# Kernel optimization log

Measured on AMD Instinct MI355X. Metric: run time of the kernel, lower is better.

The kernel has to match this reference:

```python
import jax, jax.numpy as jnp
import numpy as np

N = 100000  # num nodes


def gcn_conv(x, W, b, row, col, dinv):
    # GCNConv (default PyG): h = D^{-1/2}(A+I)D^{-1/2} (x W) + b
    h = x @ W  # [N, out]
    norm = dinv[row] * dinv[col]  # [E] symmetric normalization
    msg = h[row] * norm[:, None]  # gather + scale per edge
    agg = jax.ops.segment_sum(msg, col, num_segments=N)  # scatter-add to targets
    # self-loop contribution: norm_ii = dinv[i]^2
    agg = agg + h * (dinv * dinv)[:, None]
    return agg + b


def setup_inputs() -> dict:
    key = jax.random.key(0)
    ks = jax.random.split(key, 8)
    x = jax.random.normal(ks[0], (N, 1), dtype=jnp.float32)
    edges = jax.random.randint(ks[1], (2, 3200000), 0, N, dtype=jnp.int64)
    # glorot-ish init for weights, zeros for biases (PyG default bias init is zeros)
    W1 = jax.random.normal(ks[2], (1, 128), dtype=jnp.float32) * (1.0 / np.sqrt(1))
    b1 = jnp.zeros((128,), dtype=jnp.float32)
    W2 = jax.random.normal(ks[3], (128, 128), dtype=jnp.float32) * (1.0 / np.sqrt(128))
    b2 = jnp.zeros((128,), dtype=jnp.float32)
    Wl = jax.random.normal(ks[4], (4, 128), dtype=jnp.float32) * (1.0 / np.sqrt(128))
    bl = jnp.zeros((4,), dtype=jnp.float32)
    return {"x": x, "edges": edges, "W1": W1, "b1": b1, "W2": W2, "b2": b2, "Wl": Wl, "bl": bl}


def reference(x, edges, W1, b1, W2, b2, Wl, bl):
    row, col = edges[0], edges[1]  # source -> target
    # degree (with self loops, edge_weight=1) computed on targets
    deg = jax.ops.segment_sum(jnp.ones(row.shape[0], x.dtype), col, num_segments=N) + 1.0
    dinv = deg ** -0.5
    h = gcn_conv(x, W1, b1, row, col, dinv)
    h = jax.nn.relu(h)
    h = gcn_conv(h, W2, b2, row, col, dinv)
    h = jax.nn.relu(h)
    return h @ Wl.T + bl  # [N, 4]
```

## Files before the change

### kernel.cpp

```cpp
#include <hip/hip_runtime.h>
#include <stdint.h>

#define BK    256
#define CAP   10240
#define SLICE 1024
#define NSL   (CAP / SLICE)
#define EPE   32
#define FCH   (EPE * 256)
#define NBMAX 512

__device__ __forceinline__ float bf2f(uint16_t b){
    uint32_t u = ((uint32_t)b) << 16;
    float f; __builtin_memcpy(&f, &u, 4); return f;
}
__device__ __forceinline__ uint16_t f2bf(float f){
    uint32_t u; __builtin_memcpy(&u, &f, 4);
    uint32_t r = u + 0x7FFFu + ((u >> 16) & 1u);
    return (uint16_t)(r >> 16);
}

__global__ void k_setup(const uint32_t* __restrict__ ew, const uint16_t* __restrict__ xw,
                        const void* __restrict__ W1, const void* __restrict__ W2,
                        const void* __restrict__ b2, const void* __restrict__ Wl,
                        const void* __restrict__ bl, int* __restrict__ flg,
                        int* __restrict__ bucket_cur, int nb, float* __restrict__ g){
    int t = threadIdx.x;
    if (blockIdx.x == 0){
        __shared__ uint32_t orv;
        __shared__ int cntv;
        if (t == 0){ orv = 0u; cntv = 0; }
        __syncthreads();
        uint32_t o = 0;
        for (int i = t; i < 2048; i += 256) o |= ew[2*i + 1];
        int c = 0;
        { uint32_t e = (xw[2*t] >> 7) & 0xFFu; if (e >= 118u && e <= 130u) c = 1; }
        atomicOr(&orv, o);
        atomicAdd(&cntv, c);
        __syncthreads();
        if (t == 0){ flg[0] = (orv == 0u) ? 1 : 0; flg[1] = (cntv >= 128) ? 1 : 0; }
        for (int i = t; i < nb; i += 256) bucket_cur[i] = 0;
    } else {
        __shared__ int cntv;
        __shared__ float wp[128], wm[128];
        if (t == 0) cntv = 0;
        __syncthreads();
        int c = 0;
        { uint32_t e = (xw[2*t] >> 7) & 0xFFu; if (e >= 118u && e <= 130u) c = 1; }
        atomicAdd(&cntv, c);
        __syncthreads();
        int bf = (cntv >= 128);
        if (t < 128){
            float w1 = bf ? bf2f(((const uint16_t*)W1)[t]) : ((const float*)W1)[t];
            wp[t] = fmaxf(w1, 0.f);
            wm[t] = fmaxf(-w1, 0.f);
        }
        __syncthreads();
        if (t < 128){
            float g1 = 0.f, g2 = 0.f;
            for (int k = 0; k < 128; ++k){
                float w2 = bf ? bf2f(((const uint16_t*)W2)[k*128 + t]) : ((const float*)W2)[k*128 + t];
                g1 = fmaf(wp[k], w2, g1);
                g2 = fmaf(wm[k], w2, g2);
            }
            g[t]       = g1;
            g[128 + t] = g2;
            g[256 + t] = bf ? bf2f(((const uint16_t*)b2)[t]) : ((const float*)b2)[t];
            #pragma unroll
            for (int m = 0; m < 4; ++m)
                g[384 + m*128 + t] = bf ? bf2f(((const uint16_t*)Wl)[m*128 + t]) : ((const float*)Wl)[m*128 + t];
            if (t < 4)
                g[896 + t] = bf ? bf2f(((const uint16_t*)bl)[t]) : ((const float*)bl)[t];
        }
    }
}

__global__ void __launch_bounds__(256)
k_fill(const int* __restrict__ e32, int E, const int* __restrict__ flg,
       int* __restrict__ bucket_cur, uint32_t* __restrict__ recs, int nb){
    __shared__ int lhist[NBMAX];
    __shared__ int lbase[NBMAX];
    int tid = threadIdx.x;
    int is64 = flg[0];
    int e0 = blockIdx.x * FCH;
    int cnt = min(FCH, E - e0);
    int rr[EPE], cc[EPE];
    #pragma unroll
    for (int k = 0; k < EPE; ++k) cc[k] = -1;
    for (int i = tid; i < nb; i += 256) lhist[i] = 0;
    __syncthreads();

    if (is64 && ((E & 1) == 0) && ((cnt & 1) == 0)){
        #pragma unroll
        for (int k = 0; k < EPE/2; ++k){
            int idx = (k*256 + tid) * 2;
            if (idx < cnt){
                int4 wr = *(const int4*)&e32[2*((long)e0 + idx)];
                int4 wc = *(const int4*)&e32[2*((long)E + e0 + idx)];
                rr[2*k] = wr.x; cc[2*k] = wc.x;
                rr[2*k+1] = wr.z; cc[2*k+1] = wc.z;
            }
        }
    } else if (!is64 && ((E & 3) == 0) && ((cnt & 3) == 0)){
        #pragma unroll
        for (int k = 0; k < EPE/4; ++k){
            int idx = (k*256 + tid) * 4;
            if (idx < cnt){
                int4 wr = *(const int4*)&e32[(long)e0 + idx];
                int4 wc = *(const int4*)&e32[(long)E + e0 + idx];
                rr[4*k]   = wr.x; cc[4*k]   = wc.x;
                rr[4*k+1] = wr.y; cc[4*k+1] = wc.y;
                rr[4*k+2] = wr.z; cc[4*k+2] = wc.z;
                rr[4*k+3] = wr.w; cc[4*k+3] = wc.w;
            }
        }
    } else {
        #pragma unroll
        for (int k = 0; k < EPE; ++k){
            int i = k*256 + tid;
            if (i < cnt){
                long e = (long)e0 + i;
                if (is64){ rr[k] = e32[2*e]; cc[k] = e32[2*((long)E + e)]; }
                else     { rr[k] = e32[e];   cc[k] = e32[(long)E + e];     }
            }
        }
    }
    #pragma unroll
    for (int k = 0; k < EPE; ++k)
        if (cc[k] >= 0) atomicAdd(&lhist[cc[k] >> 8], 1);
    __syncthreads();
    for (int b = tid; b < nb; b += 256){
        int h = lhist[b];
        lbase[b] = h ? atomicAdd(&bucket_cur[b], h) : 0;
    }
    __syncthreads();
    #pragma unroll
    for (int k = 0; k < EPE; ++k){
        int c = cc[k];
        if (c >= 0){
            int b = c >> 8;
            int slot = atomicAdd(&lbase[b], 1);
            if (slot < CAP)
                recs[(long)b*CAP + slot] = (uint32_t)rr[k] | ((uint32_t)(c & 255) << 20);
        }
    }
}

__global__ void __launch_bounds__(256)
k_deg(const uint32_t* __restrict__ recs, const int* __restrict__ bucket_cur,
      int* __restrict__ degp){
    __shared__ int hist[BK];
    int bs = blockIdx.x, b = bs / NSL, s = bs - b*NSL, tid = threadIdx.x;
    hist[tid] = 0;
    __syncthreads();
    int m = min(bucket_cur[b], CAP);
    int lo = s * SLICE, hi = min(lo + SLICE, m);
    if (lo < hi){
        const uint32_t* rb = recs + (long)b*CAP;
        int i = lo + tid*4;
        uint4 w = *(const uint4*)&rb[i];
        if (i   < hi) atomicAdd(&hist[w.x >> 20], 1);
        if (i+1 < hi) atomicAdd(&hist[w.y >> 20], 1);
        if (i+2 < hi) atomicAdd(&hist[w.z >> 20], 1);
        if (i+3 < hi) atomicAdd(&hist[w.w >> 20], 1);
    }
    __syncthreads();
    degp[(long)bs*BK + tid] = hist[tid];
}

__global__ void k_node1(const int* __restrict__ degp, const void* __restrict__ x,
                        const int* __restrict__ flg, float* __restrict__ darr,
                        float* __restrict__ xdarr, int N){
    int i = blockIdx.x * blockDim.x + threadIdx.x;
    if (i >= N) return;
    int b = i >> 8, lane = i & 255;
    int cnt = 0;
    #pragma unroll
    for (int s = 0; s < NSL; ++s) cnt += degp[((long)b*NSL + s)*BK + lane];
    float d = rsqrtf((float)cnt + 1.0f);
    float xv = flg[1] ? bf2f(((const uint16_t*)x)[i]) : ((const float*)x)[i];
    darr[i]  = d;
    xdarr[i] = xv * d;
}

__global__ void __launch_bounds__(256)
k_sagg(const uint32_t* __restrict__ recs, const int* __restrict__ bucket_cur,
       const float* __restrict__ xdarr, float* __restrict__ saggp){
    __shared__ float acc[BK];
    int bs = blockIdx.x, b = bs / NSL, s = bs - b*NSL, tid = threadIdx.x;
    acc[tid] = 0.f;
    __syncthreads();
    int m = min(bucket_cur[b], CAP);
    int lo = s * SLICE, hi = min(lo + SLICE, m);
    if (lo < hi){
        const uint32_t* rb = recs + (long)b*CAP;
        int i = lo + tid*4;
        uint4 w = *(const uint4*)&rb[i];
        float v0 = xdarr[w.x & 0xFFFFFu];
        float v1 = xdarr[w.y & 0xFFFFFu];
        float v2 = xdarr[w.z & 0xFFFFFu];
        float v3 = xdarr[w.w & 0xFFFFFu];
        if (i   < hi) atomicAdd(&acc[w.x >> 20], v0);
        if (i+1 < hi) atomicAdd(&acc[w.y >> 20], v1);
        if (i+2 < hi) atomicAdd(&acc[w.z >> 20], v2);
        if (i+3 < hi) atomicAdd(&acc[w.w >> 20], v3);
    }
    __syncthreads();
    saggp[(long)bs*BK + tid] = acc[tid];
}

__global__ void k_node2(const float* __restrict__ saggp, const float* __restrict__ darr,
                        const float* __restrict__ xdarr, float2* __restrict__ pqd, int N){
    int i = blockIdx.x * blockDim.x + threadIdx.x;
    if (i >= N) return;
    int b = i >> 8, lane = i & 255;
    float sum = 0.f;
    #pragma unroll
    for (int s = 0; s < NSL; ++s) sum += saggp[((long)b*NSL + s)*BK + lane];
    float d = darr[i];
    float sv = d * (sum + xdarr[i]);
    pqd[i] = make_float2(fmaxf(sv, 0.f) * d, fmaxf(-sv, 0.f) * d);
}

__global__ void __launch_bounds__(256)
k_pq(const uint32_t* __restrict__ recs, const int* __restrict__ bucket_cur,
     const float2* __restrict__ pqd, float2* __restrict__ pqp){
    __shared__ float P[BK], Q[BK];
    int bs = blockIdx.x, b = bs / NSL, s = bs - b*NSL, tid = threadIdx.x;
    P[tid] = 0.f; Q[tid] = 0.f;
    __syncthreads();
    int m = min(bucket_cur[b], CAP);
    int lo = s * SLICE, hi = min(lo + SLICE, m);
    if (lo < hi){
        const uint32_t* rb = recs + (long)b*CAP;
        int i = lo + tid*4;
        uint4 w = *(const uint4*)&rb[i];
        float2 v0 = pqd[w.x & 0xFFFFFu];
        float2 v1 = pqd[w.y & 0xFFFFFu];
        float2 v2 = pqd[w.z & 0xFFFFFu];
        float2 v3 = pqd[w.w & 0xFFFFFu];
        if (i   < hi){ atomicAdd(&P[w.x >> 20], v0.x); atomicAdd(&Q[w.x >> 20], v0.y); }
        if (i+1 < hi){ atomicAdd(&P[w.y >> 20], v1.x); atomicAdd(&Q[w.y >> 20], v1.y); }
        if (i+2 < hi){ atomicAdd(&P[w.z >> 20], v2.x); atomicAdd(&Q[w.z >> 20], v2.y); }
        if (i+3 < hi){ atomicAdd(&P[w.w >> 20], v3.x); atomicAdd(&Q[w.w >> 20], v3.y); }
    }
    __syncthreads();
    pqp[(long)bs*BK + tid] = make_float2(P[tid], Q[tid]);
}

__global__ void __launch_bounds__(256)
k_final(const float2* __restrict__ pqp, const float* __restrict__ darr,
        const float2* __restrict__ pqd, const float* __restrict__ g,
        const int* __restrict__ flg, void* __restrict__ out, int N){
    __shared__ float G[900];
    for (int i = threadIdx.x; i < 900; i += 256) G[i] = g[i];
    __syncthreads();
    int i = blockIdx.x * blockDim.x + threadIdx.x;
    if (i >= N) return;
    int b = i >> 8, lane = i & 255;
    float P = 0.f, Q = 0.f;
    #pragma unroll
    for (int s = 0; s < NSL; ++s){
        float2 v = pqp[((long)b*NSL + s)*BK + lane];
        P += v.x; Q += v.y;
    }
    float d = darr[i];
    float2 self = pqd[i];
    float U = d * (P + self.x);
    float V = d * (Q + self.y);
    float o0 = G[896], o1 = G[897], o2 = G[898], o3 = G[899];
    #pragma unroll 4
    for (int j = 0; j < 128; ++j){
        float h = fmaxf(fmaf(U, G[j], fmaf(V, G[128 + j], G[256 + j])), 0.f);
        o0 = fmaf(h, G[384 + j], o0);
        o1 = fmaf(h, G[512 + j], o1);
        o2 = fmaf(h, G[640 + j], o2);
        o3 = fmaf(h, G[768 + j], o3);
    }
    if (flg[1]){
        uint32_t lo = (uint32_t)f2bf(o0) | ((uint32_t)f2bf(o1) << 16);
        uint32_t hi = (uint32_t)f2bf(o2) | ((uint32_t)f2bf(o3) << 16);
        ((uint2*)out)[i] = make_uint2(lo, hi);
    } else {
        ((float4*)out)[i] = make_float4(o0, o1, o2, o3);
    }
}

extern "C" void kernel_launch(void* const* d_in, const int* in_sizes, int n_in,
                              void* d_out, int out_size, void* d_ws, size_t ws_size,
                              hipStream_t stream){
    const int N = in_sizes[0];
    const int E = in_sizes[1] / 2;
    const void* x  = d_in[0];
    const int* e32 = (const int*)d_in[1];
    const void* W1 = d_in[2];
    const void* W2 = d_in[4];
    const void* b2 = d_in[5];
    const void* Wl = d_in[6];
    const void* bl = d_in[7];

    const int NB  = (N + BK - 1) / BK;
    const int nbF = (E + FCH - 1) / FCH;
    const int nb  = (N + 255) / 256;

    char* base = (char*)d_ws;
    size_t off = 0;
    auto alloc = [&](size_t bytes) -> void* {
        void* p = base + off;
        off = (off + bytes + 255) & ~(size_t)255;
        return p;
    };
    int*      flg        = (int*)     alloc(256);
    float*    g          = (float*)   alloc(1024 * 4);
    int*      bucket_cur = (int*)     alloc((size_t)NB * 4);
    float*    darr       = (float*)   alloc((size_t)N * 4);
    float*    xdarr      = (float*)   alloc((size_t)N * 4);
    float2*   pqd        = (float2*)  alloc((size_t)N * 8);
    uint32_t* recs       = (uint32_t*)alloc((size_t)NB * CAP * 4);
    int*      degp       = (int*)     alloc((size_t)NB * NSL * BK * 4);
    float*    saggp      = (float*)   alloc((size_t)NB * NSL * BK * 4);
    float2*   pqp        = (float2*)  alloc((size_t)NB * NSL * BK * 8);
    (void)ws_size; (void)n_in; (void)out_size;

    k_setup <<<2,        256, 0, stream>>>((const uint32_t*)d_in[1], (const uint16_t*)x,
                                           W1, W2, b2, Wl, bl, flg, bucket_cur, NB, g);
    k_fill  <<<nbF,      256, 0, stream>>>(e32, E, flg, bucket_cur, recs, NB);
    k_deg   <<<NB * NSL, 256, 0, stream>>>(recs, bucket_cur, degp);
    k_node1 <<<nb,       256, 0, stream>>>(degp, x, flg, darr, xdarr, N);
    k_sagg  <<<NB * NSL, 256, 0, stream>>>(recs, bucket_cur, xdarr, saggp);
    k_node2 <<<nb,       256, 0, stream>>>(saggp, darr, xdarr, pqd, N);
    k_pq    <<<NB * NSL, 256, 0, stream>>>(recs, bucket_cur, pqd, pqp);
    k_final <<<nb,       256, 0, stream>>>(pqp, darr, pqd, g, flg, d_out, N);
}
```

Measured before the change: 209.3 us.

## Regroup bucket records by source chunk and stage gathers through LDS

Adds a regroup pass that sorts each target bucket's edge records by source-node chunk of 2048 and fuses the degree histogram and dinv computation into it. The aggregation kernels then loop over source chunks, load each chunk of xdarr/pqd into shared memory and gather from LDS instead of doing random global loads. They also fold the per-slice partial sums and node epilogues into the same kernel. This drops several kernels and partial-sum buffers, but adds a full extra read/write of the records. It also serializes the work: each block handles two buckets and iterates over all 49 chunks, so parallelism drops to about 196 blocks, which may underfill the GPU.

```diff
diff --git a/kernel.cpp b/kernel.cpp
--- a/kernel.cpp
+++ b/kernel.cpp
@@ -3,11 +3,11 @@
 
 #define BK    256
 #define CAP   10240
-#define SLICE 1024
-#define NSL   (CAP / SLICE)
 #define EPE   32
 #define FCH   (EPE * 256)
 #define NBMAX 512
+#define CH    2048
+#define NQMAX 64
 
 __device__ __forceinline__ float bf2f(uint16_t b){
     uint32_t u = ((uint32_t)b) << 16;
@@ -146,142 +146,150 @@
 }
 
 __global__ void __launch_bounds__(256)
-k_deg(const uint32_t* __restrict__ recs, const int* __restrict__ bucket_cur,
-      int* __restrict__ degp){
-    __shared__ int hist[BK];
-    int bs = blockIdx.x, b = bs / NSL, s = bs - b*NSL, tid = threadIdx.x;
-    hist[tid] = 0;
+k_regroup(const uint32_t* __restrict__ recs, const int* __restrict__ bucket_cur,
+          const void* __restrict__ x, const int* __restrict__ flg,
+          uint32_t* __restrict__ recs2, int* __restrict__ binoff,
+          float* __restrict__ darr, float* __restrict__ xdarr, int N, int nq){
+    __shared__ int hist[NQMAX];
+    __shared__ int base[NQMAX + 1];
+    __shared__ int dhist[BK];
+    int b = blockIdx.x, tid = threadIdx.x;
+    if (tid < nq) hist[tid] = 0;
+    dhist[tid] = 0;
     __syncthreads();
     int m = min(bucket_cur[b], CAP);
-    int lo = s * SLICE, hi = min(lo + SLICE, m);
-    if (lo < hi){
-        const uint32_t* rb = recs + (long)b*CAP;
-        int i = lo + tid*4;
-        uint4 w = *(const uint4*)&rb[i];
-        if (i   < hi) atomicAdd(&hist[w.x >> 20], 1);
-        if (i+1 < hi) atomicAdd(&hist[w.y >> 20], 1);
-        if (i+2 < hi) atomicAdd(&hist[w.z >> 20], 1);
-        if (i+3 < hi) atomicAdd(&hist[w.w >> 20], 1);
-    }
-    __syncthreads();
-    degp[(long)bs*BK + tid] = hist[tid];
-}
-
-__global__ void k_node1(const int* __restrict__ degp, const void* __restrict__ x,
-                        const int* __restrict__ flg, float* __restrict__ darr,
-                        float* __restrict__ xdarr, int N){
-    int i = blockIdx.x * blockDim.x + threadIdx.x;
-    if (i >= N) return;
-    int b = i >> 8, lane = i & 255;
-    int cnt = 0;
-    #pragma unroll
-    for (int s = 0; s < NSL; ++s) cnt += degp[((long)b*NSL + s)*BK + lane];
-    float d = rsqrtf((float)cnt + 1.0f);
-    float xv = flg[1] ? bf2f(((const uint16_t*)x)[i]) : ((const float*)x)[i];
-    darr[i]  = d;
-    xdarr[i] = xv * d;
+    const uint32_t* rb = recs + (long)b*CAP;
+    for (int i = tid; i < m; i += 256){
+        uint32_t rec = rb[i];
+        atomicAdd(&hist[(rec & 0xFFFFFu) >> 11], 1);
+        atomicAdd(&dhist[rec >> 20], 1);
+    }
+    __syncthreads();
+    if (tid == 0){
+        int s = 0;
+        for (int q = 0; q < nq; ++q){ base[q] = s; s += hist[q]; }
+        base[nq] = s;
+    }
+    __syncthreads();
+    if (tid <= nq) binoff[b*(nq+1) + tid] = base[tid];
+    if (tid < nq)  hist[tid] = base[tid];
+    __syncthreads();
+    for (int i = tid; i < m; i += 256){
+        uint32_t rec = rb[i];
+        int slot = atomicAdd(&hist[(rec & 0xFFFFFu) >> 11], 1);
+        recs2[(long)b*CAP + slot] = rec;
+    }
+    int node = b*BK + tid;
+    if (node < N){
+        float d = rsqrtf((float)dhist[tid] + 1.0f);
+        float xv = flg[1] ? bf2f(((const uint16_t*)x)[node]) : ((const float*)x)[node];
+        darr[node]  = d;
+        xdarr[node] = xv * d;
+    }
 }
 
 __global__ void __launch_bounds__(256)
-k_sagg(const uint32_t* __restrict__ recs, const int* __restrict__ bucket_cur,
-       const float* __restrict__ xdarr, float* __restrict__ saggp){
-    __shared__ float acc[BK];
-    int bs = blockIdx.x, b = bs / NSL, s = bs - b*NSL, tid = threadIdx.x;
-    acc[tid] = 0.f;
-    __syncthreads();
-    int m = min(bucket_cur[b], CAP);
-    int lo = s * SLICE, hi = min(lo + SLICE, m);
-    if (lo < hi){
-        const uint32_t* rb = recs + (long)b*CAP;
-        int i = lo + tid*4;
-        uint4 w = *(const uint4*)&rb[i];
-        float v0 = xdarr[w.x & 0xFFFFFu];
-        float v1 = xdarr[w.y & 0xFFFFFu];
-        float v2 = xdarr[w.z & 0xFFFFFu];
-        float v3 = xdarr[w.w & 0xFFFFFu];
-        if (i   < hi) atomicAdd(&acc[w.x >> 20], v0);
-        if (i+1 < hi) atomicAdd(&acc[w.y >> 20], v1);
-        if (i+2 < hi) atomicAdd(&acc[w.z >> 20], v2);
-        if (i+3 < hi) atomicAdd(&acc[w.w >> 20], v3);
-    }
-    __syncthreads();
-    saggp[(long)bs*BK + tid] = acc[tid];
-}
-
-__global__ void k_node2(const float* __restrict__ saggp, const float* __restrict__ darr,
-                        const float* __restrict__ xdarr, float2* __restrict__ pqd, int N){
-    int i = blockIdx.x * blockDim.x + threadIdx.x;
-    if (i >= N) return;
-    int b = i >> 8, lane = i & 255;
-    float sum = 0.f;
-    #pragma unroll
-    for (int s = 0; s < NSL; ++s) sum += saggp[((long)b*NSL + s)*BK + lane];
-    float d = darr[i];
-    float sv = d * (sum + xdarr[i]);
-    pqd[i] = make_float2(fmaxf(sv, 0.f) * d, fmaxf(-sv, 0.f) * d);
+k_sagg(const uint32_t* __restrict__ recs2, const int* __restrict__ binoff,
+       const float* __restrict__ darr, const float* __restrict__ xdarr,
+       float2* __restrict__ pqd, int N, int nq, int nb){
+    __shared__ float slice[CH];
+    __shared__ float acc[2*BK];
+    int tid = threadIdx.x;
+    int b0 = blockIdx.x * 2;
+    acc[tid] = 0.f; acc[BK + tid] = 0.f;
+    for (int q = 0; q < nq; ++q){
+        __syncthreads();
+        #pragma unroll
+        for (int j = tid; j < CH; j += 256){
+            int gidx = q*CH + j;
+            slice[j] = (gidx < N) ? xdarr[gidx] : 0.f;
+        }
+        __syncthreads();
+        #pragma unroll
+        for (int bb = 0; bb < 2; ++bb){
+            int b = b0 + bb;
+            if (b >= nb) break;
+            int s0 = binoff[b*(nq+1) + q], s1 = binoff[b*(nq+1) + q + 1];
+            const uint32_t* rbase = recs2 + (long)b*CAP;
+            for (int i = s0 + tid; i < s1; i += 256){
+                uint32_t rec = rbase[i];
+                atomicAdd(&acc[bb*BK + (rec >> 20)], slice[rec & (CH-1)]);
+            }
+        }
+    }
+    __syncthreads();
+    #pragma unroll
+    for (int bb = 0; bb < 2; ++bb){
+        int node = (b0 + bb)*BK + tid;
+        if (node < N){
+            float d = darr[node];
+            float sv = d * (acc[bb*BK + tid] + xdarr[node]);
+            pqd[node] = make_float2(fmaxf(sv, 0.f) * d, fmaxf(-sv, 0.f) * d);
+        }
+    }
 }
 
 __global__ void __launch_bounds__(256)
-k_pq(const uint32_t* __restrict__ recs, const int* __restrict__ bucket_cur,
-     const float2* __restrict__ pqd, float2* __restrict__ pqp){
-    __shared__ float P[BK], Q[BK];
-    int bs = blockIdx.x, b = bs / NSL, s = bs - b*NSL, tid = threadIdx.x;
-    P[tid] = 0.f; Q[tid] = 0.f;
-    __syncthreads();
-    int m = min(bucket_cur[b], CAP);
-    int lo = s * SLICE, hi = min(lo + SLICE, m);
-    if (lo < hi){
-        const uint32_t* rb = recs + (long)b*CAP;
-        int i = lo + tid*4;
-        uint4 w = *(const uint4*)&rb[i];
-        float2 v0 = pqd[w.x & 0xFFFFFu];
-        float2 v1 = pqd[w.y & 0xFFFFFu];
-        float2 v2 = pqd[w.z & 0xFFFFFu];
-        float2 v3 = pqd[w.w & 0xFFFFFu];
-        if (i   < hi){ atomicAdd(&P[w.x >> 20], v0.x); atomicAdd(&Q[w.x >> 20], v0.y); }
-        if (i+1 < hi){ atomicAdd(&P[w.y >> 20], v1.x); atomicAdd(&Q[w.y >> 20], v1.y); }
-        if (i+2 < hi){ atomicAdd(&P[w.z >> 20], v2.x); atomicAdd(&Q[w.z >> 20], v2.y); }
-        if (i+3 < hi){ atomicAdd(&P[w.w >> 20], v3.x); atomicAdd(&Q[w.w >> 20], v3.y); }
-    }
-    __syncthreads();
-    pqp[(long)bs*BK + tid] = make_float2(P[tid], Q[tid]);
-}
-
-__global__ void __launch_bounds__(256)
-k_final(const float2* __restrict__ pqp, const float* __restrict__ darr,
-        const float2* __restrict__ pqd, const float* __restrict__ g,
-        const int* __restrict__ flg, void* __restrict__ out, int N){
+k_pqfin(const uint32_t* __restrict__ recs2, const int* __restrict__ binoff,
+        const float* __restrict__ darr, const float2* __restrict__ pqd,
+        const float* __restrict__ g, const int* __restrict__ flg,
+        void* __restrict__ out, int N, int nq, int nb){
+    __shared__ float2 slice[CH];
+    __shared__ float P[2*BK], Q[2*BK];
     __shared__ float G[900];
-    for (int i = threadIdx.x; i < 900; i += 256) G[i] = g[i];
-    __syncthreads();
-    int i = blockIdx.x * blockDim.x + threadIdx.x;
-    if (i >= N) return;
-    int b = i >> 8, lane = i & 255;
-    float P = 0.f, Q = 0.f;
-    #pragma unroll
-    for (int s = 0; s < NSL; ++s){
-        float2 v = pqp[((long)b*NSL + s)*BK + lane];
-        P += v.x; Q += v.y;
-    }
-    float d = darr[i];
-    float2 self = pqd[i];
-    float U = d * (P + self.x);
-    float V = d * (Q + self.y);
-    float o0 = G[896], o1 = G[897], o2 = G[898], o3 = G[899];
-    #pragma unroll 4
-    for (int j = 0; j < 128; ++j){
-        float h = fmaxf(fmaf(U, G[j], fmaf(V, G[128 + j], G[256 + j])), 0.f);
-        o0 = fmaf(h, G[384 + j], o0);
-        o1 = fmaf(h, G[512 + j], o1);
-        o2 = fmaf(h, G[640 + j], o2);
-        o3 = fmaf(h, G[768 + j], o3);
-    }
-    if (flg[1]){
-        uint32_t lo = (uint32_t)f2bf(o0) | ((uint32_t)f2bf(o1) << 16);
-        uint32_t hi = (uint32_t)f2bf(o2) | ((uint32_t)f2bf(o3) << 16);
-        ((uint2*)out)[i] = make_uint2(lo, hi);
-    } else {
-        ((float4*)out)[i] = make_float4(o0, o1, o2, o3);
+    int tid = threadIdx.x;
+    int b0 = blockIdx.x * 2;
+    P[tid] = 0.f; P[BK+tid] = 0.f; Q[tid] = 0.f; Q[BK+tid] = 0.f;
+    for (int i = tid; i < 900; i += 256) G[i] = g[i];
+    for (int q = 0; q < nq; ++q){
+        __syncthreads();
+        #pragma unroll
+        for (int j = tid; j < CH; j += 256){
+            int gidx = q*CH + j;
+            slice[j] = (gidx < N) ? pqd[gidx] : make_float2(0.f, 0.f);
+        }
+        __syncthreads();
+        #pragma unroll
+        for (int bb = 0; bb < 2; ++bb){
+            int b = b0 + bb;
+            if (b >= nb) break;
+            int s0 = binoff[b*(nq+1) + q], s1 = binoff[b*(nq+1) + q + 1];
+            const uint32_t* rbase = recs2 + (long)b*CAP;
+            for (int i = s0 + tid; i < s1; i += 256){
+                uint32_t rec = rbase[i];
+                float2 v = slice[rec & (CH-1)];
+                int cl = bb*BK + (rec >> 20);
+                atomicAdd(&P[cl], v.x);
+                atomicAdd(&Q[cl], v.y);
+            }
+        }
+    }
+    __syncthreads();
+    #pragma unroll
+    for (int bb = 0; bb < 2; ++bb){
+        int node = (b0 + bb)*BK + tid;
+        if (node < N){
+            float d = darr[node];
+            float2 self = pqd[node];
+            float U = d * (P[bb*BK + tid] + self.x);
+            float V = d * (Q[bb*BK + tid] + self.y);
+            float o0 = G[896], o1 = G[897], o2 = G[898], o3 = G[899];
+            #pragma unroll 4
+            for (int j = 0; j < 128; ++j){
+                float h = fmaxf(fmaf(U, G[j], fmaf(V, G[128 + j], G[256 + j])), 0.f);
+                o0 = fmaf(h, G[384 + j], o0);
+                o1 = fmaf(h, G[512 + j], o1);
+                o2 = fmaf(h, G[640 + j], o2);
+                o3 = fmaf(h, G[768 + j], o3);
+            }
+            if (flg[1]){
+                uint32_t lo = (uint32_t)f2bf(o0) | ((uint32_t)f2bf(o1) << 16);
+                uint32_t hi = (uint32_t)f2bf(o2) | ((uint32_t)f2bf(o3) << 16);
+                ((uint2*)out)[node] = make_uint2(lo, hi);
+            } else {
+                ((float4*)out)[node] = make_float4(o0, o1, o2, o3);
+            }
+        }
     }
 }
 
@@ -300,7 +308,7 @@
 
     const int NB  = (N + BK - 1) / BK;
     const int nbF = (E + FCH - 1) / FCH;
-    const int nb  = (N + 255) / 256;
+    const int nq  = (N + CH - 1) / CH;
 
     char* base = (char*)d_ws;
     size_t off = 0;
@@ -316,18 +324,15 @@
     float*    xdarr      = (float*)   alloc((size_t)N * 4);
     float2*   pqd        = (float2*)  alloc((size_t)N * 8);
     uint32_t* recs       = (uint32_t*)alloc((size_t)NB * CAP * 4);
-    int*      degp       = (int*)     alloc((size_t)NB * NSL * BK * 4);
-    float*    saggp      = (float*)   alloc((size_t)NB * NSL * BK * 4);
-    float2*   pqp        = (float2*)  alloc((size_t)NB * NSL * BK * 8);
+    uint32_t* recs2      = (uint32_t*)alloc((size_t)NB * CAP * 4);
+    int*      binoff     = (int*)     alloc((size_t)NB * (nq+1) * 4);
     (void)ws_size; (void)n_in; (void)out_size;
 
-    k_setup <<<2,        256, 0, stream>>>((const uint32_t*)d_in[1], (const uint16_t*)x,
-                                           W1, W2, b2, Wl, bl, flg, bucket_cur, NB, g);
-    k_fill  <<<nbF,      256, 0, stream>>>(e32, E, flg, bucket_cur, recs, NB);
-    k_deg   <<<NB * NSL, 256, 0, stream>>>(recs, bucket_cur, degp);
-    k_node1 <<<nb,       256, 0, stream>>>(degp, x, flg, darr, xdarr, N);
-    k_sagg  <<<NB * NSL, 256, 0, stream>>>(recs, bucket_cur, xdarr, saggp);
-    k_node2 <<<nb,       256, 0, stream>>>(saggp, darr, xdarr, pqd, N);
-    k_pq    <<<NB * NSL, 256, 0, stream>>>(recs, bucket_cur, pqd, pqp);
-    k_final <<<nb,       256, 0, stream>>>(pqp, darr, pqd, g, flg, d_out, N);
-}
+    k_setup   <<<2,          256, 0, stream>>>((const uint32_t*)d_in[1], (const uint16_t*)x,
+                                               W1, W2, b2, Wl, bl, flg, bucket_cur, NB, g);
+    k_fill    <<<nbF,        256, 0, stream>>>(e32, E, flg, bucket_cur, recs, NB);
+    k_regroup <<<NB,         256, 0, stream>>>(recs, bucket_cur, x, flg, recs2, binoff,
+                                               darr, xdarr, N, nq);
+    k_sagg    <<<(NB+1)/2,   256, 0, stream>>>(recs2, binoff, darr, xdarr, pqd, N, nq, NB);
+    k_pqfin   <<<(NB+1)/2,   256, 0, stream>>>(recs2, binoff, darr, pqd, g, flg, d_out, N, nq, NB);
+}
```

Measured after the change: 443.9 us. +112.1%, slower.

## Use fixed-point 64-bit LDS atomics, double slice size, split histograms

Applied to the files above, without the earlier changes.

Doubles the per-block slice so each thread handles 8 edge records loaded with nontemporal 128-bit loads, halving the block count. The float LDS atomics in the aggregation kernels become integer 64-bit atomics on fixed-point values, and in the P/Q kernel both channels are packed into one 64-bit atomic. Accumulators are split into two copies by thread parity to reduce LDS contention. The fixed-point scaling adds quantization error and a risk of overflow in the packed 32-bit P/Q fields, and the changed summation can alter numerics.

```diff
diff --git a/kernel.cpp b/kernel.cpp
--- a/kernel.cpp
+++ b/kernel.cpp
@@ -3,12 +3,22 @@
 
 #define BK    256
 #define CAP   10240
-#define SLICE 1024
+#define SLICE 2048
 #define NSL   (CAP / SLICE)
 #define EPE   32
 #define FCH   (EPE * 256)
 #define NBMAX 512
 
+#define SC_S  16777216.0f
+#define ISC_S (1.0f/16777216.0f)
+#define SC_P  65536.0f
+#define ISC_P (1.0f/65536.0f)
+
+typedef __attribute__((ext_vector_type(4))) unsigned int u32x4;
+
+__device__ __forceinline__ u32x4 ntload4(const uint32_t* p){
+    return __builtin_nontemporal_load((const u32x4*)p);
+}
 __device__ __forceinline__ float bf2f(uint16_t b){
     uint32_t u = ((uint32_t)b) << 16;
     float f; __builtin_memcpy(&f, &u, 4); return f;
@@ -148,23 +158,27 @@
 __global__ void __launch_bounds__(256)
 k_deg(const uint32_t* __restrict__ recs, const int* __restrict__ bucket_cur,
       int* __restrict__ degp){
-    __shared__ int hist[BK];
+    __shared__ int hist[2][BK];
     int bs = blockIdx.x, b = bs / NSL, s = bs - b*NSL, tid = threadIdx.x;
-    hist[tid] = 0;
+    hist[0][tid] = 0; hist[1][tid] = 0;
     __syncthreads();
     int m = min(bucket_cur[b], CAP);
     int lo = s * SLICE, hi = min(lo + SLICE, m);
     if (lo < hi){
         const uint32_t* rb = recs + (long)b*CAP;
-        int i = lo + tid*4;
-        uint4 w = *(const uint4*)&rb[i];
-        if (i   < hi) atomicAdd(&hist[w.x >> 20], 1);
-        if (i+1 < hi) atomicAdd(&hist[w.y >> 20], 1);
-        if (i+2 < hi) atomicAdd(&hist[w.z >> 20], 1);
-        if (i+3 < hi) atomicAdd(&hist[w.w >> 20], 1);
-    }
-    __syncthreads();
-    degp[(long)bs*BK + tid] = hist[tid];
+        int i = lo + tid*8;
+        u32x4 w0 = ntload4(rb + i);
+        u32x4 w1 = ntload4(rb + i + 4);
+        int h = tid & 1;
+        #pragma unroll
+        for (int e = 0; e < 4; ++e)
+            if (i + e < hi) atomicAdd(&hist[h][w0[e] >> 20], 1);
+        #pragma unroll
+        for (int e = 0; e < 4; ++e)
+            if (i + 4 + e < hi) atomicAdd(&hist[h][w1[e] >> 20], 1);
+    }
+    __syncthreads();
+    degp[(long)bs*BK + tid] = hist[0][tid] + hist[1][tid];
 }
 
 __global__ void k_node1(const int* __restrict__ degp, const void* __restrict__ x,
@@ -185,27 +199,33 @@
 __global__ void __launch_bounds__(256)
 k_sagg(const uint32_t* __restrict__ recs, const int* __restrict__ bucket_cur,
        const float* __restrict__ xdarr, float* __restrict__ saggp){
-    __shared__ float acc[BK];
+    __shared__ unsigned long long acc[2][BK];
     int bs = blockIdx.x, b = bs / NSL, s = bs - b*NSL, tid = threadIdx.x;
-    acc[tid] = 0.f;
+    acc[0][tid] = 0ull; acc[1][tid] = 0ull;
     __syncthreads();
     int m = min(bucket_cur[b], CAP);
     int lo = s * SLICE, hi = min(lo + SLICE, m);
     if (lo < hi){
         const uint32_t* rb = recs + (long)b*CAP;
-        int i = lo + tid*4;
-        uint4 w = *(const uint4*)&rb[i];
-        float v0 = xdarr[w.x & 0xFFFFFu];
-        float v1 = xdarr[w.y & 0xFFFFFu];
-        float v2 = xdarr[w.z & 0xFFFFFu];
-        float v3 = xdarr[w.w & 0xFFFFFu];
-        if (i   < hi) atomicAdd(&acc[w.x >> 20], v0);
-        if (i+1 < hi) atomicAdd(&acc[w.y >> 20], v1);
-        if (i+2 < hi) atomicAdd(&acc[w.z >> 20], v2);
-        if (i+3 < hi) atomicAdd(&acc[w.w >> 20], v3);
-    }
-    __syncthreads();
-    saggp[(long)bs*BK + tid] = acc[tid];
+        int i = lo + tid*8;
+        u32x4 w0 = ntload4(rb + i);
+        u32x4 w1 = ntload4(rb + i + 4);
+        int h = tid & 1;
+        uint32_t rec[8] = {w0[0], w0[1], w0[2], w0[3], w1[0], w1[1], w1[2], w1[3]};
+        float v[8];
+        #pragma unroll
+        for (int e = 0; e < 8; ++e) v[e] = xdarr[rec[e] & 0xFFFFFu];
+        #pragma unroll
+        for (int e = 0; e < 8; ++e){
+            if (i + e < hi){
+                long long q = (long long)(v[e] * SC_S);
+                atomicAdd(&acc[h][rec[e] >> 20], (unsigned long long)q);
+            }
+        }
+    }
+    __syncthreads();
+    long long t = (long long)(acc[0][tid] + acc[1][tid]);
+    saggp[(long)bs*BK + tid] = (float)t * ISC_S;
 }
 
 __global__ void k_node2(const float* __restrict__ saggp, const float* __restrict__ darr,
@@ -224,27 +244,37 @@
 __global__ void __launch_bounds__(256)
 k_pq(const uint32_t* __restrict__ recs, const int* __restrict__ bucket_cur,
      const float2* __restrict__ pqd, float2* __restrict__ pqp){
-    __shared__ float P[BK], Q[BK];
+    __shared__ unsigned long long acc[2][BK];
     int bs = blockIdx.x, b = bs / NSL, s = bs - b*NSL, tid = threadIdx.x;
-    P[tid] = 0.f; Q[tid] = 0.f;
+    acc[0][tid] = 0ull; acc[1][tid] = 0ull;
     __syncthreads();
     int m = min(bucket_cur[b], CAP);
     int lo = s * SLICE, hi = min(lo + SLICE, m);
     if (lo < hi){
         const uint32_t* rb = recs + (long)b*CAP;
-        int i = lo + tid*4;
-        uint4 w = *(const uint4*)&rb[i];
-        float2 v0 = pqd[w.x & 0xFFFFFu];
-        float2 v1 = pqd[w.y & 0xFFFFFu];
-        float2 v2 = pqd[w.z & 0xFFFFFu];
-        float2 v3 = pqd[w.w & 0xFFFFFu];
-        if (i   < hi){ atomicAdd(&P[w.x >> 20], v0.x); atomicAdd(&Q[w.x >> 20], v0.y); }
-        if (i+1 < hi){ atomicAdd(&P[w.y >> 20], v1.x); atomicAdd(&Q[w.y >> 20], v1.y); }
-        if (i+2 < hi){ atomicAdd(&P[w.z >> 20], v2.x); atomicAdd(&Q[w.z >> 20], v2.y); }
-        if (i+3 < hi){ atomicAdd(&P[w.w >> 20], v3.x); atomicAdd(&Q[w.w >> 20], v3.y); }
-    }
-    __syncthreads();
-    pqp[(long)bs*BK + tid] = make_float2(P[tid], Q[tid]);
+        int i = lo + tid*8;
+        u32x4 w0 = ntload4(rb + i);
+        u32x4 w1 = ntload4(rb + i + 4);
+        int h = tid & 1;
+        uint32_t rec[8] = {w0[0], w0[1], w0[2], w0[3], w1[0], w1[1], w1[2], w1[3]};
+        float2 v[8];
+        #pragma unroll
+        for (int e = 0; e < 8; ++e) v[e] = pqd[rec[e] & 0xFFFFFu];
+        #pragma unroll
+        for (int e = 0; e < 8; ++e){
+            if (i + e < hi){
+                uint32_t pi = (uint32_t)(v[e].x * SC_P + 0.5f);
+                uint32_t qi = (uint32_t)(v[e].y * SC_P + 0.5f);
+                unsigned long long pk = ((unsigned long long)pi << 32) | (unsigned long long)qi;
+                atomicAdd(&acc[h][rec[e] >> 20], pk);
+            }
+        }
+    }
+    __syncthreads();
+    unsigned long long t = acc[0][tid] + acc[1][tid];
+    float P = (float)(uint32_t)(t >> 32) * ISC_P;
+    float Q = (float)(uint32_t)(t & 0xFFFFFFFFull) * ISC_P;
+    pqp[(long)bs*BK + tid] = make_float2(P, Q);
 }
 
 __global__ void __launch_bounds__(256)
```

After: 172.7 us. 17.5% less time.
